# Kernel tuning notes

Hardware: AMD Instinct MI355X
Metric: run time of the kernel (lower is better)

## Reference

```python
import jax, jax.numpy as jnp
import numpy as np

HOP = 240  # subsample stride from torch.arange(239, T, 240)

def _causal_conv(x, w, b):
    # x: [B, Cin, T], w: [Cout, Cin, K], b: [Cout]
    pad = w.shape[-1] - 1
    xp = jnp.pad(x, ((0, 0), (0, 0), (pad, 0)))
    y = jax.lax.conv_general_dilated(xp, w, window_strides=(1,), padding='VALID',
                                     dimension_numbers=('NCW', 'OIW', 'NCW'))
    return y + b[None, :, None], xp[:, :, -pad:]

def _rvq(z, codebooks):
    # z: [B, T, D]; codebooks: [n, codebook_size, cd] with D = n*cd
    B, T, D = z.shape
    n, cs, cd = codebooks.shape
    zc = z.reshape(B, T, n, cd)
    r = zc[:, :, 0, :]
    qs, idxs = [], []
    for i in range(n):  # fixed small loop over 8 codebooks (sequential residual chain)
        cb = codebooks[i]  # [cs, cd]
        dist = (r ** 2).sum(-1, keepdims=True) + (cb ** 2).sum(-1) \
               - 2.0 * jnp.einsum('btd,cd->btc', r, cb)
        idx = jnp.argmin(dist, axis=-1)  # [B, T]
        q = cb[idx]                      # [B, T, cd]
        idxs.append(idx)
        qs.append(q)
        if i < n - 1:
            r = zc[:, :, i + 1, :] + (r - q)
    z_q = jnp.stack(qs, axis=2).reshape(B, T, D)
    return z_q, jnp.stack(idxs, axis=1)  # indices: [B, n, T]

def setup_inputs() -> dict:
    key = jax.random.key(0)
    ks = jax.random.split(key, 12)
    B, T = 4, 72000
    d_model = 512
    n_cb, cb_size, cb_dim = 8, 1024, d_model // 8
    s = 0.05
    return {
        'audio':   jax.random.normal(ks[0], (B, 1, T), dtype=jnp.float32),
        'conv1_w': jax.random.normal(ks[1], (64, 1, 7), dtype=jnp.float32) * s,
        'conv1_b': jnp.zeros((64,), dtype=jnp.float32),
        'conv2_w': jax.random.normal(ks[2], (128, 64, 5), dtype=jnp.float32) * s,
        'conv2_b': jnp.zeros((128,), dtype=jnp.float32),
        'conv3_w': jax.random.normal(ks[3], (256, 128, 5), dtype=jnp.float32) * s,
        'conv3_b': jnp.zeros((256,), dtype=jnp.float32),
        'conv4_w': jax.random.normal(ks[4], (d_model, 256, 3), dtype=jnp.float32) * s,
        'conv4_b': jnp.zeros((d_model,), dtype=jnp.float32),
        'codebooks': jax.random.normal(ks[5], (n_cb, cb_size, cb_dim), dtype=jnp.float32),
        'head_w': jax.random.normal(ks[6], (4, 64, d_model), dtype=jnp.float32) * s,
        'head_b': jnp.zeros((4, 64), dtype=jnp.float32),
    }

def reference(audio, conv1_w, conv1_b, conv2_w, conv2_b, conv3_w, conv3_b,
              conv4_w, conv4_b, codebooks, head_w, head_b):
    x, s1 = _causal_conv(audio, conv1_w, conv1_b); x = jax.nn.elu(x)
    x, s2 = _causal_conv(x, conv2_w, conv2_b);     x = jax.nn.elu(x)
    x, s3 = _causal_conv(x, conv3_w, conv3_b);     x = jax.nn.elu(x)
    x, s4 = _causal_conv(x, conv4_w, conv4_b);     x = jax.nn.elu(x)
    idx = jnp.arange(HOP - 1, x.shape[-1], HOP)
    x_sub = jnp.take(x, idx, axis=-1)              # [B, D, T_sub]
    z_q, a_tokens = _rvq(jnp.transpose(x_sub, (0, 2, 1)), codebooks)
    # b_logits: [B, 4, T_sub, 64]
    b_logits = jnp.einsum('btd,hod->bhto', z_q, head_w) + head_b[None, :, None, :]
    return a_tokens, b_logits, s1, s2, s3, s4
```

## Files before the change

kernel.cpp:

```cpp
#include <hip/hip_runtime.h>
#include <math.h>

#define HOP   240
#define T_IN  72000
#define NB    4
#define NF    300
#define NCB   8
#define CBS   1024
#define CBD   64

#define OFF_LOG 9600
#define OFF_S1  316800
#define OFF_S2  316824
#define OFF_S3  317848
#define OFF_S4  319896

#define WS_NRM   0
#define WS_W2P4  8192
#define WS_W3P4  49152
#define WS_W4P4  212992
#define WS_HW4   606208
#define WS_CBP4  737280
#define WS_TOTAL 1261568ull

__device__ __forceinline__ float elu1(float x) { return x > 0.f ? x : expm1f(x); }
__device__ __forceinline__ float dot4(float4 a, float4 b) {
    return a.x * b.x + a.y * b.y + a.z * b.z + a.w * b.w;
}
__device__ __forceinline__ float red16(float v) {
    v += __shfl_xor(v, 1); v += __shfl_xor(v, 2);
    v += __shfl_xor(v, 4); v += __shfl_xor(v, 8);
    return v;
}
__device__ __forceinline__ unsigned int fkey(float f) {
    unsigned int u = __float_as_uint(f);
    return (u & 0x80000000u) ? ~u : (u | 0x80000000u);
}

__global__ __launch_bounds__(256)
void prep_kernel(const float* __restrict__ w2, const float* __restrict__ w3,
                 const float* __restrict__ w4, const float* __restrict__ hw,
                 const float* __restrict__ cbs, float* __restrict__ wsf)
{
    const int bid = blockIdx.x;
    const float* src; float* dst;
    int C, I, K, c0, i0;
    bool do_norm = false; float* nrmp = nullptr;
    if (bid < 2)       { src = w2; dst = wsf + WS_W2P4; C = 128;  I = 64;  K = 5; c0 = bid * 64;        i0 = 0; }
    else if (bid < 10) { const int e = bid - 2;  src = w3; dst = wsf + WS_W3P4; C = 256;  I = 128; K = 5; c0 = (e >> 1) * 64; i0 = (e & 1) * 64; }
    else if (bid < 42) { const int e = bid - 10; src = w4; dst = wsf + WS_W4P4; C = 512;  I = 256; K = 3; c0 = (e >> 2) * 64; i0 = (e & 3) * 64; }
    else if (bid < 74) { const int e = bid - 42; src = hw; dst = wsf + WS_HW4;  C = 256;  I = 512; K = 1; c0 = (e & 3) * 64;  i0 = (e >> 2) * 64; }
    else {
        const int e = bid - 74, book = e >> 4;
        src = cbs + (size_t)book * 65536; dst = wsf + WS_CBP4 + (size_t)book * 65536;
        C = 1024; I = 64; K = 1; c0 = (e & 15) * 64; i0 = 0;
        do_norm = true; nrmp = wsf + WS_NRM + book * 1024;
    }
    const int L = I * K;
    const int lane = threadIdx.x & 63, q = threadIdx.x >> 6;

    __shared__ float tS[64][65];
    __shared__ float npart[4][64];

    for (int k = 0; k < K; ++k) {
        #pragma unroll
        for (int r = 0; r < 16; ++r) {
            const int cl = q * 16 + r;
            tS[cl][lane] = src[(size_t)(c0 + cl) * L + (i0 + lane) * K + k];
        }
        __syncthreads();
        if (do_norm && k == 0) {
            float s = 0.f;
            #pragma unroll
            for (int j = 0; j < 16; ++j) { const float v = tS[lane][q * 16 + j]; s += v * v; }
            npart[q][lane] = s;
        }
        #pragma unroll
        for (int jj = 0; jj < 4; ++jj) {
            const int j = q * 4 + jj;
            float4 v;
            v.x = tS[lane][4 * j + 0];
            v.y = tS[lane][4 * j + 1];
            v.z = tS[lane][4 * j + 2];
            v.w = tS[lane][4 * j + 3];
            ((float4*)dst)[(size_t)(k * (I >> 2) + (i0 >> 2) + j) * C + (c0 + lane)] = v;
        }
        __syncthreads();
    }
    if (do_norm && threadIdx.x < 64)
        nrmp[c0 + threadIdx.x] = npart[0][threadIdx.x] + npart[1][threadIdx.x]
                               + npart[2][threadIdx.x] + npart[3][threadIdx.x];
}

__global__ __launch_bounds__(512, 4)
void mega_kernel(const float* __restrict__ audio,
                 const float* __restrict__ w1, const float* __restrict__ b1,
                 const float* __restrict__ b2, const float* __restrict__ b3,
                 const float* __restrict__ b4, const float* __restrict__ cbs,
                 const float* __restrict__ hb, const float* __restrict__ wsf,
                 float* __restrict__ out)
{
    const int blk = blockIdx.x;
    const int b   = blk / 100;
    const int fi  = blk - b * 100;
    const int f0  = fi * 3;
    const bool tail = (fi == 99);
    const int tid = threadIdx.x;
    const int lane = tid & 63, wid = tid >> 6;

    __shared__ float ashL[3][18];
    __shared__ __align__(16) float y1L[3 * 704];
    __shared__ __align__(16) float y2L[3 * 896];
    __shared__ __align__(16) float y3L[3 * 768];
    __shared__ __align__(16) float zsL[3 * 512];
    __shared__ __align__(16) float zqL[3 * 512];
    __shared__ __align__(16) float rs[192];
    __shared__ float redL[2688];
    __shared__ float rnS[3];
    __shared__ unsigned long long mk[2][3];

    if (tid < 51) {
        const int f = tid / 17, j = tid - f * 17;
        ashL[f][j] = audio[b * T_IN + (f0 + f) * HOP + 223 + j];
    }
    if (tail && tid < 6) out[OFF_S1 + b * 6 + tid] = audio[b * T_IN + (T_IN - 6) + tid];
    if (tid < 6) mk[tid / 3][tid % 3] = ~0ull;
    __syncthreads();

    if (tid < 192) {
        const int f = tid >> 6, o = tid & 63;
        float wv[7];
        #pragma unroll
        for (int k = 0; k < 7; ++k) wv[k] = w1[o * 7 + k];
        const float bias = b1[o];
        float y1r[11];
        #pragma unroll
        for (int p = 0; p < 11; ++p) {
            float a = bias;
            #pragma unroll
            for (int k = 0; k < 7; ++k) a += wv[k] * ashL[f][p + k];
            y1r[p] = elu1(a);
            y1L[f * 704 + p * 64 + o] = y1r[p];
        }
        if (tail && f == 2) {
            #pragma unroll
            for (int j = 0; j < 4; ++j) out[OFF_S2 + b * 256 + o * 4 + j] = y1r[7 + j];
        }
    }
    __syncthreads();

    {
        const int c = tid & 127, h = (tid >> 7) & 1, g = tid >> 8;
        const int fb = g * 2, nf = g ? 1 : 2;
        float acc[2][7];
        #pragma unroll
        for (int ff = 0; ff < 2; ++ff)
            #pragma unroll
            for (int p = 0; p < 7; ++p) acc[ff][p] = 0.f;

        const float4* wq = (const float4*)(wsf + WS_W2P4);
        for (int it = 0; it < 8; ++it) {
            const int itg = h * 8 + it;
            float4 wv[5];
            #pragma unroll
            for (int k = 0; k < 5; ++k) wv[k] = wq[(k * 16 + itg) * 128 + c];
            #pragma unroll
            for (int q = 0; q < 11; ++q) {
                float4 xv[2];
                #pragma unroll
                for (int ff = 0; ff < 2; ++ff)
                    if (ff < nf) xv[ff] = *(const float4*)&y1L[(fb + ff) * 704 + q * 64 + itg * 4];
                #pragma unroll
                for (int k = 0; k < 5; ++k) {
                    const int p = q - k;
                    if (p < 0 || p > 6) continue;
                    #pragma unroll
                    for (int ff = 0; ff < 2; ++ff)
                        if (ff < nf) acc[ff][p] += dot4(wv[k], xv[ff]);
                }
            }
        }
        if (h == 1) {
            #pragma unroll
            for (int ff = 0; ff < 2; ++ff)
                if (ff < nf)
                    #pragma unroll
                    for (int p = 0; p < 7; ++p)
                        redL[((fb + ff) * 7 + p) * 128 + c] = acc[ff][p];
        }
        __syncthreads();
        if (h == 0) {
            const float bias = b2[c];
            #pragma unroll
            for (int ff = 0; ff < 2; ++ff)
                if (ff < nf) {
                    const int f = fb + ff;
                    #pragma unroll
                    for (int p = 0; p < 7; ++p) {
                        const float v = elu1(acc[ff][p] + redL[(f * 7 + p) * 128 + c] + bias);
                        y2L[f * 896 + p * 128 + c] = v;
                        if (tail && f == 2 && p >= 3)
                            out[OFF_S3 + b * 512 + c * 4 + (p - 3)] = v;
                    }
                }
        }
        __syncthreads();
    }

    {
        const int c = tid & 255, h = tid >> 8;
        float acc[3][3];
        #pragma unroll
        for (int ff = 0; ff < 3; ++ff) { acc[ff][0] = acc[ff][1] = acc[ff][2] = 0.f; }

        const float4* wq = (const float4*)(wsf + WS_W3P4);
        for (int it = 0; it < 16; ++it) {
            const int itg = h * 16 + it;
            float4 wv[5];
            #pragma unroll
            for (int k = 0; k < 5; ++k) wv[k] = wq[(k * 32 + itg) * 256 + c];
            #pragma unroll
            for (int q = 0; q < 7; ++q) {
                float4 xv[3];
                #pragma unroll
                for (int ff = 0; ff < 3; ++ff)
                    xv[ff] = *(const float4*)&y2L[ff * 896 + q * 128 + itg * 4];
                #pragma unroll
                for (int k = 0; k < 5; ++k) {
                    const int p = q - k;
                    if (p < 0 || p > 2) continue;
                    #pragma unroll
                    for (int ff = 0; ff < 3; ++ff) acc[ff][p] += dot4(wv[k], xv[ff]);
                }
            }
        }
        if (h == 1) {
            #pragma unroll
            for (int ff = 0; ff < 3; ++ff)
                #pragma unroll
                for (int p = 0; p < 3; ++p) redL[(ff * 3 + p) * 256 + c] = acc[ff][p];
        }
        __syncthreads();
        if (h == 0) {
            const float bias = b3[c];
            #pragma unroll
            for (int ff = 0; ff < 3; ++ff)
                #pragma unroll
                for (int p = 0; p < 3; ++p) {
                    const float v = elu1(acc[ff][p] + redL[(ff * 3 + p) * 256 + c] + bias);
                    y3L[ff * 768 + p * 256 + c] = v;
                    if (tail && ff == 2 && p >= 1)
                        out[OFF_S4 + b * 512 + c * 2 + (p - 1)] = v;
                }
        }
        __syncthreads();
    }

    {
        const int c = tid;
        float acc[3] = {0.f, 0.f, 0.f};
        const float4* wq = (const float4*)(wsf + WS_W4P4);
        for (int rc = 0; rc < 192; ++rc) {
            const float4 w0 = wq[rc * 512 + c];
            #pragma unroll
            for (int ff = 0; ff < 3; ++ff) {
                const float4 xv = *(const float4*)&y3L[ff * 768 + rc * 4];
                acc[ff] += dot4(w0, xv);
            }
        }
        const float bias = b4[c];
        #pragma unroll
        for (int ff = 0; ff < 3; ++ff)
            zsL[ff * 512 + c] = elu1(acc[ff] + bias);
    }
    __syncthreads();

    if (tid < 192) {
        const float v = zsL[wid * 512 + lane];
        rs[tid] = v;
        float ss = v * v;
        #pragma unroll
        for (int m = 1; m < 64; m <<= 1) ss += __shfl_xor(ss, m);
        if (lane == 0) rnS[wid] = ss;
    }
    __syncthreads();

    const int c0 = tid << 1;
    for (int s = 0; s < NCB; ++s) {
        const float4* cbq = (const float4*)(wsf + WS_CBP4) + (size_t)s * 16384;
        float dA[3], dB[3];
        #pragma unroll
        for (int ff = 0; ff < 3; ++ff) { dA[ff] = 0.f; dB[ff] = 0.f; }

        for (int dc = 0; dc < 16; ++dc) {
            const float4 la = cbq[dc * 1024 + c0];
            const float4 lb = cbq[dc * 1024 + c0 + 1];
            #pragma unroll
            for (int ff = 0; ff < 3; ++ff) {
                const float4 rv = *(const float4*)&rs[ff * 64 + dc * 4];
                dA[ff] += dot4(la, rv);
                dB[ff] += dot4(lb, rv);
            }
        }
        const float2 nn = *(const float2*)(wsf + WS_NRM + s * CBS + c0);
        unsigned long long key[3];
        #pragma unroll
        for (int ff = 0; ff < 3; ++ff) {
            const float rn = rnS[ff];
            const float da = (rn + nn.x) - 2.f * dA[ff];
            const float db = (rn + nn.y) - 2.f * dB[ff];
            const unsigned long long ka = ((unsigned long long)fkey(da) << 32) | (unsigned)c0;
            const unsigned long long kb = ((unsigned long long)fkey(db) << 32) | (unsigned)(c0 + 1);
            key[ff] = ka < kb ? ka : kb;
        }
        #pragma unroll
        for (int m = 1; m < 64; m <<= 1) {
            #pragma unroll
            for (int ff = 0; ff < 3; ++ff) {
                const unsigned long long o = __shfl_xor(key[ff], m);
                if (o < key[ff]) key[ff] = o;
            }
        }
        if (lane == 0) {
            #pragma unroll
            for (int ff = 0; ff < 3; ++ff) atomicMin(&mk[s & 1][ff], key[ff]);
        }
        __syncthreads();

        if (tid < 3)
            out[b * (NCB * NF) + s * NF + (f0 + tid)]
                = (float)(unsigned)(mk[s & 1][tid] & 0xFFFFFFFFull);
        if (tid < 192) {
            const int idx = (int)(unsigned)(mk[s & 1][wid] & 0xFFFFFFFFull);
            const float qv = cbs[(size_t)(s * CBS + idx) * CBD + lane];
            zqL[wid * 512 + s * 64 + lane] = qv;
            if (s < NCB - 1) {
                const float nr = zsL[wid * 512 + (s + 1) * 64 + lane] + (rs[tid] - qv);
                rs[tid] = nr;
                float ss = nr * nr;
                #pragma unroll
                for (int m = 1; m < 64; m <<= 1) ss += __shfl_xor(ss, m);
                if (lane == 0) rnS[wid] = ss;
            }
        }
        if (tid >= 192 && tid < 195) mk[(s + 1) & 1][tid - 192] = ~0ull;
        __syncthreads();
    }

    {
        const int oc = tid & 255, h = tid >> 8;
        const float4* hq = (const float4*)(wsf + WS_HW4);
        float acc[3] = {0.f, 0.f, 0.f};
        for (int rc = 0; rc < 64; ++rc) {
            const float4 wv = hq[(h * 64 + rc) * 256 + oc];
            #pragma unroll
            for (int ff = 0; ff < 3; ++ff) {
                const float4 xv = *(const float4*)&zqL[ff * 512 + h * 256 + rc * 4];
                acc[ff] += dot4(wv, xv);
            }
        }
        if (h == 1) {
            #pragma unroll
            for (int ff = 0; ff < 3; ++ff) redL[oc * 3 + ff] = acc[ff];
        }
        __syncthreads();
        if (h == 0) {
            const float bias = hb[oc];
            const int hh = oc >> 6, o = oc & 63;
            #pragma unroll
            for (int ff = 0; ff < 3; ++ff)
                out[OFF_LOG + ((size_t)(b * 4 + hh) * NF + (f0 + ff)) * 64 + o]
                    = acc[ff] + redL[oc * 3 + ff] + bias;
        }
    }
}

__global__ __launch_bounds__(256)
void enc_fused_kernel(const float* __restrict__ audio,
                      const float* __restrict__ w1, const float* __restrict__ b1,
                      const float* __restrict__ w2, const float* __restrict__ b2,
                      const float* __restrict__ w3, const float* __restrict__ b3,
                      const float* __restrict__ w4, const float* __restrict__ b4,
                      const float* __restrict__ cbs,
                      const float* __restrict__ hw, const float* __restrict__ hb,
                      float* __restrict__ out)
{
    const int tid = threadIdx.x;
    const int g = tid >> 4, sub = tid & 15, j0 = sub << 2;
    const int bf = blockIdx.x, b = bf / NF, f = bf - b * NF;
    const int t = f * HOP + (HOP - 1);

    __shared__ __align__(16) float ash[17];
    __shared__ __align__(16) float y1s[11 * 64];
    __shared__ __align__(16) float y2s[7 * 128];
    __shared__ __align__(16) float y3s[3 * 256];
    __shared__ __align__(16) float in_l[2240];
    __shared__ __align__(16) float zs[512];
    __shared__ __align__(16) float zqs[512];
    __shared__ __align__(16) float rsl[64];
    __shared__ float rdd[16]; __shared__ int rdi[16]; __shared__ int bidx_s;

    if (tid < 17) ash[tid] = audio[b * T_IN + (t - 16) + tid];
    __syncthreads();
    for (int j = tid; j < 11 * 64; j += 256) {
        const int p = j >> 6, o = j & 63;
        float acc = b1[o];
        for (int k = 0; k < 7; ++k) acc += w1[o * 7 + k] * ash[p + k];
        y1s[p * 64 + o] = elu1(acc);
    }
    __syncthreads();
    for (int j = tid; j < 7 * 320; j += 256) {
        const int p = j / 320, r = j - p * 320, i = r / 5, k = r - i * 5;
        in_l[j] = y1s[(p + k) * 64 + i];
    }
    __syncthreads();
    {
        float a[7];
        for (int ch = 0; ch < 8; ++ch) {
            const int c = g + (ch << 4);
            const float* wr = w2 + c * 320;
            for (int p = 0; p < 7; ++p) a[p] = 0.f;
            for (int st = 0; st < 5; ++st) {
                const float4 wv = *(const float4*)(wr + st * 64 + j0);
                for (int p = 0; p < 7; ++p)
                    a[p] += dot4(wv, *(const float4*)&in_l[p * 320 + st * 64 + j0]);
            }
            for (int p = 0; p < 7; ++p) a[p] = red16(a[p]);
            if (sub == 0) for (int p = 0; p < 7; ++p) y2s[p * 128 + c] = elu1(a[p] + b2[c]);
        }
    }
    __syncthreads();
    for (int j = tid; j < 3 * 640; j += 256) {
        const int p = j / 640, r = j - p * 640, i = r / 5, k = r - i * 5;
        in_l[j] = y2s[(p + k) * 128 + i];
    }
    __syncthreads();
    {
        float a[3];
        for (int ch = 0; ch < 16; ++ch) {
            const int c = g + (ch << 4);
            const float* wr = w3 + c * 640;
            a[0] = a[1] = a[2] = 0.f;
            for (int st = 0; st < 10; ++st) {
                const float4 wv = *(const float4*)(wr + st * 64 + j0);
                for (int p = 0; p < 3; ++p)
                    a[p] += dot4(wv, *(const float4*)&in_l[p * 640 + st * 64 + j0]);
            }
            for (int p = 0; p < 3; ++p) a[p] = red16(a[p]);
            if (sub == 0) for (int p = 0; p < 3; ++p) y3s[p * 256 + c] = elu1(a[p] + b3[c]);
        }
    }
    __syncthreads();
    for (int j = tid; j < 768; j += 256) { const int i = j / 3, k = j - i * 3; in_l[j] = y3s[k * 256 + i]; }
    __syncthreads();
    for (int ch = 0; ch < 32; ++ch) {
        const int c = g + (ch << 4);
        const float* wr = w4 + c * 768;
        float a = 0.f;
        for (int st = 0; st < 12; ++st)
            a += dot4(*(const float4*)(wr + st * 64 + j0), *(const float4*)&in_l[st * 64 + j0]);
        a = red16(a);
        if (sub == 0) zs[c] = elu1(a + b4[c]);
    }
    __syncthreads();
    if (tid < 64) rsl[tid] = zs[tid];
    __syncthreads();
    for (int s = 0; s < NCB; ++s) {
        const float* cb = cbs + s * (CBS * CBD);
        const float4 rv = *(const float4*)(rsl + j0);
        const float rn = red16(dot4(rv, rv));
        float bestd = 3.402823466e38f; int besti = 0;
        const int cc0 = g * 64;
        for (int cc = 0; cc < 64; ++cc) {
            const int c = cc0 + cc;
            const float4 cv = *(const float4*)(cb + c * CBD + j0);
            const float dt = red16(dot4(cv, rv));
            const float nnv = red16(dot4(cv, cv));
            const float d = rn + nnv - 2.f * dt;
            if (d < bestd) { bestd = d; besti = c; }
        }
        if (sub == 0) { rdd[g] = bestd; rdi[g] = besti; }
        __syncthreads();
        if (tid == 0) {
            float bd = rdd[0]; int bi = rdi[0];
            for (int q = 1; q < 16; ++q) if (rdd[q] < bd) { bd = rdd[q]; bi = rdi[q]; }
            bidx_s = bi;
            out[b * (NCB * NF) + s * NF + f] = (float)bi;
        }
        __syncthreads();
        const int idx = bidx_s;
        if (g == 0) {
            const float4 q4 = *(const float4*)(cb + idx * CBD + j0);
            *(float4*)&zqs[s * 64 + j0] = q4;
            if (s < NCB - 1) {
                const float4 zn = *(const float4*)&zs[(s + 1) * 64 + j0];
                float4 nr;
                nr.x = zn.x + (rv.x - q4.x); nr.y = zn.y + (rv.y - q4.y);
                nr.z = zn.z + (rv.z - q4.z); nr.w = zn.w + (rv.w - q4.w);
                *(float4*)&rsl[j0] = nr;
            }
        }
        __syncthreads();
    }
    for (int oo = 0; oo < 16; ++oo) {
        const int oc = g + (oo << 4);
        const float* wr = hw + oc * 512;
        float a = 0.f;
        for (int st = 0; st < 8; ++st)
            a += dot4(*(const float4*)(wr + st * 64 + j0), *(const float4*)&zqs[st * 64 + j0]);
        a = red16(a);
        if (sub == 0) {
            const int h = oc >> 6, o = oc & 63;
            out[OFF_LOG + ((b * 4 + h) * NF + f) * 64 + o] = a + hb[oc];
        }
    }
    if (f == NF - 1) {
        if (tid < 6) out[OFF_S1 + b * 6 + tid] = audio[b * T_IN + (T_IN - 6) + tid];
        out[OFF_S2 + b * 256 + tid] = y1s[(7 + (tid & 3)) * 64 + (tid >> 2)];
        for (int j = tid; j < 512; j += 256)
            out[OFF_S3 + b * 512 + j] = y2s[(3 + (j & 3)) * 128 + (j >> 2)];
        for (int j = tid; j < 512; j += 256)
            out[OFF_S4 + b * 512 + j] = y3s[(1 + (j & 1)) * 256 + (j >> 1)];
    }
}

extern "C" void kernel_launch(void* const* d_in, const int* in_sizes, int n_in,
                              void* d_out, int out_size, void* d_ws, size_t ws_size,
                              hipStream_t stream) {
    const float* audio = (const float*)d_in[0];
    const float* w1 = (const float*)d_in[1];
    const float* b1 = (const float*)d_in[2];
    const float* w2 = (const float*)d_in[3];
    const float* b2 = (const float*)d_in[4];
    const float* w3 = (const float*)d_in[5];
    const float* b3 = (const float*)d_in[6];
    const float* w4 = (const float*)d_in[7];
    const float* b4 = (const float*)d_in[8];
    const float* cbs = (const float*)d_in[9];
    const float* hw = (const float*)d_in[10];
    const float* hb = (const float*)d_in[11];
    float* out = (float*)d_out;
    float* wsf = (float*)d_ws;

    if (ws_size >= WS_TOTAL * sizeof(float)) {
        prep_kernel<<<dim3(202), 256, 0, stream>>>(w2, w3, w4, hw, cbs, wsf);
        mega_kernel<<<dim3(400), 512, 0, stream>>>(audio, w1, b1, b2, b3, b4,
                                                   cbs, hb, wsf, out);
    } else {
        enc_fused_kernel<<<dim3(NB * NF), 256, 0, stream>>>(
            audio, w1, b1, w2, b2, w3, b3, w4, b4, cbs, hw, hb, out);
    }
}
```

Baseline: 245.3 us.

## Split work finer: two frames per block, per-tap prep blocks, float argmin

The main kernel now processes two frames per block instead of three, raising the grid from 400 to 600 blocks so more of the GPU's compute units are busy. The prep kernel launches one block per kernel tap instead of looping over taps, giving 306 blocks. The RVQ argmin reduction is reworked to shuffle float minima and then resolve the index with a ballot, instead of shuffling 64-bit packed keys. The trade-off is that each weight load is now reused across fewer frames, which raises total weight traffic from L2.

```diff
diff --git a/kernel.cpp b/kernel.cpp
--- a/kernel.cpp
+++ b/kernel.cpp
@@ -44,16 +44,30 @@
 {
     const int bid = blockIdx.x;
     const float* src; float* dst;
-    int C, I, K, c0, i0;
+    int C, I, K, c0, i0, k;
     bool do_norm = false; float* nrmp = nullptr;
-    if (bid < 2)       { src = w2; dst = wsf + WS_W2P4; C = 128;  I = 64;  K = 5; c0 = bid * 64;        i0 = 0; }
-    else if (bid < 10) { const int e = bid - 2;  src = w3; dst = wsf + WS_W3P4; C = 256;  I = 128; K = 5; c0 = (e >> 1) * 64; i0 = (e & 1) * 64; }
-    else if (bid < 42) { const int e = bid - 10; src = w4; dst = wsf + WS_W4P4; C = 512;  I = 256; K = 3; c0 = (e >> 2) * 64; i0 = (e & 3) * 64; }
-    else if (bid < 74) { const int e = bid - 42; src = hw; dst = wsf + WS_HW4;  C = 256;  I = 512; K = 1; c0 = (e & 3) * 64;  i0 = (e >> 2) * 64; }
-    else {
-        const int e = bid - 74, book = e >> 4;
+    if (bid < 10) {
+        const int e = bid;
+        src = w2; dst = wsf + WS_W2P4; C = 128; I = 64; K = 5;
+        c0 = (e / 5) * 64; i0 = 0; k = e % 5;
+    } else if (bid < 50) {
+        const int e = bid - 10;
+        src = w3; dst = wsf + WS_W3P4; C = 256; I = 128; K = 5;
+        const int t = e / 5; k = e % 5;
+        c0 = (t >> 1) * 64; i0 = (t & 1) * 64;
+    } else if (bid < 146) {
+        const int e = bid - 50;
+        src = w4; dst = wsf + WS_W4P4; C = 512; I = 256; K = 3;
+        const int t = e / 3; k = e % 3;
+        c0 = (t >> 2) * 64; i0 = (t & 3) * 64;
+    } else if (bid < 178) {
+        const int e = bid - 146;
+        src = hw; dst = wsf + WS_HW4; C = 256; I = 512; K = 1;
+        c0 = (e & 3) * 64; i0 = (e >> 2) * 64; k = 0;
+    } else {
+        const int e = bid - 178, book = e >> 4;
         src = cbs + (size_t)book * 65536; dst = wsf + WS_CBP4 + (size_t)book * 65536;
-        C = 1024; I = 64; K = 1; c0 = (e & 15) * 64; i0 = 0;
+        C = 1024; I = 64; K = 1; c0 = (e & 15) * 64; i0 = 0; k = 0;
         do_norm = true; nrmp = wsf + WS_NRM + book * 1024;
     }
     const int L = I * K;
@@ -62,34 +76,34 @@
     __shared__ float tS[64][65];
     __shared__ float npart[4][64];
 
-    for (int k = 0; k < K; ++k) {
-        #pragma unroll
-        for (int r = 0; r < 16; ++r) {
-            const int cl = q * 16 + r;
-            tS[cl][lane] = src[(size_t)(c0 + cl) * L + (i0 + lane) * K + k];
-        }
-        __syncthreads();
-        if (do_norm && k == 0) {
-            float s = 0.f;
-            #pragma unroll
-            for (int j = 0; j < 16; ++j) { const float v = tS[lane][q * 16 + j]; s += v * v; }
-            npart[q][lane] = s;
-        }
-        #pragma unroll
-        for (int jj = 0; jj < 4; ++jj) {
-            const int j = q * 4 + jj;
-            float4 v;
-            v.x = tS[lane][4 * j + 0];
-            v.y = tS[lane][4 * j + 1];
-            v.z = tS[lane][4 * j + 2];
-            v.w = tS[lane][4 * j + 3];
-            ((float4*)dst)[(size_t)(k * (I >> 2) + (i0 >> 2) + j) * C + (c0 + lane)] = v;
-        }
-        __syncthreads();
-    }
-    if (do_norm && threadIdx.x < 64)
-        nrmp[c0 + threadIdx.x] = npart[0][threadIdx.x] + npart[1][threadIdx.x]
-                               + npart[2][threadIdx.x] + npart[3][threadIdx.x];
+    #pragma unroll
+    for (int r = 0; r < 16; ++r) {
+        const int cl = q * 16 + r;
+        tS[cl][lane] = src[(size_t)(c0 + cl) * L + (i0 + lane) * K + k];
+    }
+    __syncthreads();
+
+    if (do_norm) {
+        float s = 0.f;
+        #pragma unroll
+        for (int j = 0; j < 16; ++j) { const float v = tS[lane][q * 16 + j]; s += v * v; }
+        npart[q][lane] = s;
+        __syncthreads();
+        if (threadIdx.x < 64)
+            nrmp[c0 + threadIdx.x] = npart[0][threadIdx.x] + npart[1][threadIdx.x]
+                                   + npart[2][threadIdx.x] + npart[3][threadIdx.x];
+    }
+
+    #pragma unroll
+    for (int jj = 0; jj < 4; ++jj) {
+        const int j = q * 4 + jj;
+        float4 v;
+        v.x = tS[lane][4 * j + 0];
+        v.y = tS[lane][4 * j + 1];
+        v.z = tS[lane][4 * j + 2];
+        v.w = tS[lane][4 * j + 3];
+        ((float4*)dst)[(size_t)(k * (I >> 2) + (i0 >> 2) + j) * C + (c0 + lane)] = v;
+    }
 }
 
 __global__ __launch_bounds__(512, 4)
@@ -101,33 +115,33 @@
                  float* __restrict__ out)
 {
     const int blk = blockIdx.x;
-    const int b   = blk / 100;
-    const int fi  = blk - b * 100;
-    const int f0  = fi * 3;
-    const bool tail = (fi == 99);
+    const int b   = blk / 150;
+    const int fi  = blk - b * 150;
+    const int f0  = fi * 2;
+    const bool tail = (fi == 149);
     const int tid = threadIdx.x;
     const int lane = tid & 63, wid = tid >> 6;
 
-    __shared__ float ashL[3][18];
-    __shared__ __align__(16) float y1L[3 * 704];
-    __shared__ __align__(16) float y2L[3 * 896];
-    __shared__ __align__(16) float y3L[3 * 768];
-    __shared__ __align__(16) float zsL[3 * 512];
-    __shared__ __align__(16) float zqL[3 * 512];
-    __shared__ __align__(16) float rs[192];
-    __shared__ float redL[2688];
-    __shared__ float rnS[3];
-    __shared__ unsigned long long mk[2][3];
-
-    if (tid < 51) {
+    __shared__ float ashL[2][18];
+    __shared__ __align__(16) float y1L[2 * 704];
+    __shared__ __align__(16) float y2L[2 * 896];
+    __shared__ __align__(16) float y3L[2 * 768];
+    __shared__ __align__(16) float zsL[2 * 512];
+    __shared__ __align__(16) float zqL[2 * 512];
+    __shared__ __align__(16) float rs[128];
+    __shared__ float redL[1792];
+    __shared__ float rnS[2];
+    __shared__ unsigned long long mk[2][2];
+
+    if (tid < 34) {
         const int f = tid / 17, j = tid - f * 17;
         ashL[f][j] = audio[b * T_IN + (f0 + f) * HOP + 223 + j];
     }
     if (tail && tid < 6) out[OFF_S1 + b * 6 + tid] = audio[b * T_IN + (T_IN - 6) + tid];
-    if (tid < 6) mk[tid / 3][tid % 3] = ~0ull;
-    __syncthreads();
-
-    if (tid < 192) {
+    if (tid < 4) mk[tid >> 1][tid & 1] = ~0ull;
+    __syncthreads();
+
+    if (tid < 128) {
         const int f = tid >> 6, o = tid & 63;
         float wv[7];
         #pragma unroll
@@ -142,7 +156,7 @@
             y1r[p] = elu1(a);
             y1L[f * 704 + p * 64 + o] = y1r[p];
         }
-        if (tail && f == 2) {
+        if (tail && f == 1) {
             #pragma unroll
             for (int j = 0; j < 4; ++j) out[OFF_S2 + b * 256 + o * 4 + j] = y1r[7 + j];
         }
@@ -150,13 +164,10 @@
     __syncthreads();
 
     {
-        const int c = tid & 127, h = (tid >> 7) & 1, g = tid >> 8;
-        const int fb = g * 2, nf = g ? 1 : 2;
-        float acc[2][7];
-        #pragma unroll
-        for (int ff = 0; ff < 2; ++ff)
-            #pragma unroll
-            for (int p = 0; p < 7; ++p) acc[ff][p] = 0.f;
+        const int c = tid & 127, h = (tid >> 7) & 1, f = tid >> 8;
+        float acc[7];
+        #pragma unroll
+        for (int p = 0; p < 7; ++p) acc[p] = 0.f;
 
         const float4* wq = (const float4*)(wsf + WS_W2P4);
         for (int it = 0; it < 8; ++it) {
@@ -166,52 +177,39 @@
             for (int k = 0; k < 5; ++k) wv[k] = wq[(k * 16 + itg) * 128 + c];
             #pragma unroll
             for (int q = 0; q < 11; ++q) {
-                float4 xv[2];
-                #pragma unroll
-                for (int ff = 0; ff < 2; ++ff)
-                    if (ff < nf) xv[ff] = *(const float4*)&y1L[(fb + ff) * 704 + q * 64 + itg * 4];
+                const float4 xv = *(const float4*)&y1L[f * 704 + q * 64 + itg * 4];
                 #pragma unroll
                 for (int k = 0; k < 5; ++k) {
                     const int p = q - k;
                     if (p < 0 || p > 6) continue;
-                    #pragma unroll
-                    for (int ff = 0; ff < 2; ++ff)
-                        if (ff < nf) acc[ff][p] += dot4(wv[k], xv[ff]);
+                    acc[p] += dot4(wv[k], xv);
                 }
             }
         }
         if (h == 1) {
             #pragma unroll
-            for (int ff = 0; ff < 2; ++ff)
-                if (ff < nf)
-                    #pragma unroll
-                    for (int p = 0; p < 7; ++p)
-                        redL[((fb + ff) * 7 + p) * 128 + c] = acc[ff][p];
+            for (int p = 0; p < 7; ++p)
+                redL[(f * 7 + p) * 128 + c] = acc[p];
         }
         __syncthreads();
         if (h == 0) {
             const float bias = b2[c];
             #pragma unroll
-            for (int ff = 0; ff < 2; ++ff)
-                if (ff < nf) {
-                    const int f = fb + ff;
-                    #pragma unroll
-                    for (int p = 0; p < 7; ++p) {
-                        const float v = elu1(acc[ff][p] + redL[(f * 7 + p) * 128 + c] + bias);
-                        y2L[f * 896 + p * 128 + c] = v;
-                        if (tail && f == 2 && p >= 3)
-                            out[OFF_S3 + b * 512 + c * 4 + (p - 3)] = v;
-                    }
-                }
+            for (int p = 0; p < 7; ++p) {
+                const float v = elu1(acc[p] + redL[(f * 7 + p) * 128 + c] + bias);
+                y2L[f * 896 + p * 128 + c] = v;
+                if (tail && f == 1 && p >= 3)
+                    out[OFF_S3 + b * 512 + c * 4 + (p - 3)] = v;
+            }
         }
         __syncthreads();
     }
 
     {
         const int c = tid & 255, h = tid >> 8;
-        float acc[3][3];
-        #pragma unroll
-        for (int ff = 0; ff < 3; ++ff) { acc[ff][0] = acc[ff][1] = acc[ff][2] = 0.f; }
+        float acc[2][3];
+        #pragma unroll
+        for (int ff = 0; ff < 2; ++ff) { acc[ff][0] = acc[ff][1] = acc[ff][2] = 0.f; }
 
         const float4* wq = (const float4*)(wsf + WS_W3P4);
         for (int it = 0; it < 16; ++it) {
@@ -221,22 +219,22 @@
             for (int k = 0; k < 5; ++k) wv[k] = wq[(k * 32 + itg) * 256 + c];
             #pragma unroll
             for (int q = 0; q < 7; ++q) {
-                float4 xv[3];
+                float4 xv[2];
                 #pragma unroll
-                for (int ff = 0; ff < 3; ++ff)
+                for (int ff = 0; ff < 2; ++ff)
                     xv[ff] = *(const float4*)&y2L[ff * 896 + q * 128 + itg * 4];
                 #pragma unroll
                 for (int k = 0; k < 5; ++k) {
                     const int p = q - k;
                     if (p < 0 || p > 2) continue;
                     #pragma unroll
-                    for (int ff = 0; ff < 3; ++ff) acc[ff][p] += dot4(wv[k], xv[ff]);
+                    for (int ff = 0; ff < 2; ++ff) acc[ff][p] += dot4(wv[k], xv[ff]);
                 }
             }
         }
         if (h == 1) {
             #pragma unroll
-            for (int ff = 0; ff < 3; ++ff)
+            for (int ff = 0; ff < 2; ++ff)
                 #pragma unroll
                 for (int p = 0; p < 3; ++p) redL[(ff * 3 + p) * 256 + c] = acc[ff][p];
         }
@@ -244,12 +242,12 @@
         if (h == 0) {
             const float bias = b3[c];
             #pragma unroll
-            for (int ff = 0; ff < 3; ++ff)
+            for (int ff = 0; ff < 2; ++ff)
                 #pragma unroll
                 for (int p = 0; p < 3; ++p) {
                     const float v = elu1(acc[ff][p] + redL[(ff * 3 + p) * 256 + c] + bias);
                     y3L[ff * 768 + p * 256 + c] = v;
-                    if (tail && ff == 2 && p >= 1)
+                    if (tail && ff == 1 && p >= 1)
                         out[OFF_S4 + b * 512 + c * 2 + (p - 1)] = v;
                 }
         }
@@ -258,24 +256,24 @@
 
     {
         const int c = tid;
-        float acc[3] = {0.f, 0.f, 0.f};
+        float acc[2] = {0.f, 0.f};
         const float4* wq = (const float4*)(wsf + WS_W4P4);
         for (int rc = 0; rc < 192; ++rc) {
             const float4 w0 = wq[rc * 512 + c];
             #pragma unroll
-            for (int ff = 0; ff < 3; ++ff) {
+            for (int ff = 0; ff < 2; ++ff) {
                 const float4 xv = *(const float4*)&y3L[ff * 768 + rc * 4];
                 acc[ff] += dot4(w0, xv);
             }
         }
         const float bias = b4[c];
         #pragma unroll
-        for (int ff = 0; ff < 3; ++ff)
+        for (int ff = 0; ff < 2; ++ff)
             zsL[ff * 512 + c] = elu1(acc[ff] + bias);
     }
     __syncthreads();
 
-    if (tid < 192) {
+    if (tid < 128) {
         const float v = zsL[wid * 512 + lane];
         rs[tid] = v;
         float ss = v * v;
@@ -288,49 +286,45 @@
     const int c0 = tid << 1;
     for (int s = 0; s < NCB; ++s) {
         const float4* cbq = (const float4*)(wsf + WS_CBP4) + (size_t)s * 16384;
-        float dA[3], dB[3];
-        #pragma unroll
-        for (int ff = 0; ff < 3; ++ff) { dA[ff] = 0.f; dB[ff] = 0.f; }
+        float dA[2] = {0.f, 0.f}, dB[2] = {0.f, 0.f};
 
         for (int dc = 0; dc < 16; ++dc) {
             const float4 la = cbq[dc * 1024 + c0];
             const float4 lb = cbq[dc * 1024 + c0 + 1];
             #pragma unroll
-            for (int ff = 0; ff < 3; ++ff) {
+            for (int ff = 0; ff < 2; ++ff) {
                 const float4 rv = *(const float4*)&rs[ff * 64 + dc * 4];
                 dA[ff] += dot4(la, rv);
                 dB[ff] += dot4(lb, rv);
             }
         }
         const float2 nn = *(const float2*)(wsf + WS_NRM + s * CBS + c0);
-        unsigned long long key[3];
-        #pragma unroll
-        for (int ff = 0; ff < 3; ++ff) {
+        #pragma unroll
+        for (int ff = 0; ff < 2; ++ff) {
             const float rn = rnS[ff];
             const float da = (rn + nn.x) - 2.f * dA[ff];
             const float db = (rn + nn.y) - 2.f * dB[ff];
-            const unsigned long long ka = ((unsigned long long)fkey(da) << 32) | (unsigned)c0;
-            const unsigned long long kb = ((unsigned long long)fkey(db) << 32) | (unsigned)(c0 + 1);
-            key[ff] = ka < kb ? ka : kb;
-        }
-        #pragma unroll
-        for (int m = 1; m < 64; m <<= 1) {
-            #pragma unroll
-            for (int ff = 0; ff < 3; ++ff) {
-                const unsigned long long o = __shfl_xor(key[ff], m);
-                if (o < key[ff]) key[ff] = o;
-            }
-        }
-        if (lane == 0) {
-            #pragma unroll
-            for (int ff = 0; ff < 3; ++ff) atomicMin(&mk[s & 1][ff], key[ff]);
-        }
-        __syncthreads();
-
-        if (tid < 3)
+            float bestd = da; int besti = c0;
+            if (db < da) { bestd = db; besti = c0 + 1; }
+            float m0 = bestd;
+            #pragma unroll
+            for (int m = 1; m < 64; m <<= 1) {
+                const float o = __shfl_xor(m0, m);
+                m0 = fminf(m0, o);
+            }
+            const unsigned long long mask = __ballot(bestd == m0);
+            const int lowlane = __ffsll((long long)mask) - 1;
+            const int widx = __shfl(besti, lowlane);
+            if (lane == 0)
+                atomicMin(&mk[s & 1][ff],
+                          ((unsigned long long)fkey(m0) << 32) | (unsigned)widx);
+        }
+        __syncthreads();
+
+        if (tid < 2)
             out[b * (NCB * NF) + s * NF + (f0 + tid)]
                 = (float)(unsigned)(mk[s & 1][tid] & 0xFFFFFFFFull);
-        if (tid < 192) {
+        if (tid < 128) {
             const int idx = (int)(unsigned)(mk[s & 1][wid] & 0xFFFFFFFFull);
             const float qv = cbs[(size_t)(s * CBS + idx) * CBD + lane];
             zqL[wid * 512 + s * 64 + lane] = qv;
@@ -343,34 +337,34 @@
                 if (lane == 0) rnS[wid] = ss;
             }
         }
-        if (tid >= 192 && tid < 195) mk[(s + 1) & 1][tid - 192] = ~0ull;
+        if (tid >= 128 && tid < 130) mk[(s + 1) & 1][tid - 128] = ~0ull;
         __syncthreads();
     }
 
     {
         const int oc = tid & 255, h = tid >> 8;
         const float4* hq = (const float4*)(wsf + WS_HW4);
-        float acc[3] = {0.f, 0.f, 0.f};
+        float acc[2] = {0.f, 0.f};
         for (int rc = 0; rc < 64; ++rc) {
             const float4 wv = hq[(h * 64 + rc) * 256 + oc];
             #pragma unroll
-            for (int ff = 0; ff < 3; ++ff) {
+            for (int ff = 0; ff < 2; ++ff) {
                 const float4 xv = *(const float4*)&zqL[ff * 512 + h * 256 + rc * 4];
                 acc[ff] += dot4(wv, xv);
             }
         }
         if (h == 1) {
             #pragma unroll
-            for (int ff = 0; ff < 3; ++ff) redL[oc * 3 + ff] = acc[ff];
+            for (int ff = 0; ff < 2; ++ff) redL[oc * 2 + ff] = acc[ff];
         }
         __syncthreads();
         if (h == 0) {
             const float bias = hb[oc];
             const int hh = oc >> 6, o = oc & 63;
             #pragma unroll
-            for (int ff = 0; ff < 3; ++ff)
+            for (int ff = 0; ff < 2; ++ff)
                 out[OFF_LOG + ((size_t)(b * 4 + hh) * NF + (f0 + ff)) * 64 + o]
-                    = acc[ff] + redL[oc * 3 + ff] + bias;
+                    = acc[ff] + redL[oc * 2 + ff] + bias;
         }
     }
 }
@@ -543,8 +537,8 @@
     float* wsf = (float*)d_ws;
 
     if (ws_size >= WS_TOTAL * sizeof(float)) {
-        prep_kernel<<<dim3(202), 256, 0, stream>>>(w2, w3, w4, hw, cbs, wsf);
-        mega_kernel<<<dim3(400), 512, 0, stream>>>(audio, w1, b1, b2, b3, b4,
+        prep_kernel<<<dim3(306), 256, 0, stream>>>(w2, w3, w4, hw, cbs, wsf);
+        mega_kernel<<<dim3(600), 512, 0, stream>>>(audio, w1, b1, b2, b3, b4,
                                                    cbs, hb, wsf, out);
     } else {
         enc_fused_kernel<<<dim3(NB * NF), 256, 0, stream>>>(
```

New measurement: 564.7 us. +130.2%, slower.
